# Performance work log

Measured on AMD Instinct MI355X. Metric: run time of the kernel, lower is better.

The kernel has to match this reference:

```python
import jax, jax.numpy as jnp
import numpy as np

EPS = 1e-12  # torch F.normalize clamps the norm at 1e-12

def _l2norm(v, axis):
    n = jnp.sqrt(jnp.sum(v * v, axis=axis, keepdims=True))
    return v / jnp.maximum(n, EPS)

def setup_inputs() -> dict:
    key = jax.random.key(0)
    k1, k2, k3, k4 = jax.random.split(key, 4)
    N, C, H, W, K = 64, 64, 64, 64, 128
    alpha = 1.0
    x = jax.random.normal(k1, (N, C, H, W), dtype=jnp.float32)
    centroids = jax.random.uniform(k2, (K, C), dtype=jnp.float32)
    # conv is initialized from centroids (2*alpha*c, -alpha*||c||) but is an
    # independent parameter after init; keep the init relationship for realism.
    conv_w = 2.0 * alpha * centroids
    conv_b = -alpha * jnp.sqrt(jnp.sum(centroids * centroids, axis=1))
    return {"x": x, "centroids": centroids, "conv_w": conv_w, "conv_b": conv_b}

def reference(x, centroids, conv_w, conv_b):
    N, C, H, W = x.shape
    K = centroids.shape[0]
    # L2-normalize descriptors along channel dim
    xn = _l2norm(x, axis=1)                                   # [N,C,H,W]
    # 1x1 conv == per-pixel linear map C->K
    logits = jnp.einsum('nchw,kc->nkhw', xn, conv_w) + conv_b[None, :, None, None]
    sa = jax.nn.softmax(logits.reshape(N, K, H * W), axis=1)  # [N,K,HW]
    xf = xn.reshape(N, C, H * W)                              # [N,C,HW]
    # vlad[n,k,c] = sum_l sa[n,k,l] * (xf[n,c,l] - centroids[k,c])
    #            = (sa @ xf^T)[n,k,c] - sum_l sa[n,k,l] * centroids[k,c]
    vlad = jnp.einsum('nkl,ncl->nkc', sa, xf) - sa.sum(axis=-1)[:, :, None] * centroids[None]
    vlad = _l2norm(vlad, axis=2)            # intra-normalization per cluster
    vlad = vlad.reshape(N, K * C)
    vlad = _l2norm(vlad, axis=1)            # global L2 normalization
    return vlad
```

## Files before the change

### kernel.cpp

```cpp
#include <hip/hip_runtime.h>
#include <math.h>

#define NIMG   64
#define CDIM   64
#define HWPX   4096
#define KCL    128
#define TL     64
#define SHIFT  10.0f
#define RSQRT128 0.08838834764831845f

#define XP_S 72
#define XC_S 72
#define PH_S 72

typedef __attribute__((ext_vector_type(8))) short short8;
typedef __attribute__((ext_vector_type(4))) float f32x4;

#define MFMA(a, b, c) __builtin_amdgcn_mfma_f32_16x16x32_bf16((a), (b), (c), 0, 0, 0)

#define PERM_HI16 0x07060302u

#define BAR() do {                                          \
    asm volatile("s_waitcnt lgkmcnt(0)" ::: "memory");      \
    __builtin_amdgcn_s_barrier();                           \
    __builtin_amdgcn_sched_barrier(0);                      \
} while (0)

template <int NP>
__global__ __launch_bounds__(256, 2)
void netvlad_main(const float* __restrict__ x,
                  const float* __restrict__ conv_w,
                  const float* __restrict__ conv_b,
                  float* __restrict__ vout,
                  float* __restrict__ asout,
                  int use_atomic)
{
    constexpr int PIXPART = HWPX / NP;
    constexpr int NCHUNK  = PIXPART / TL;

    __shared__ __align__(16) short xp_hi[2][TL * XP_S], xp_lo[2][TL * XP_S];
    __shared__ __align__(16) short xc[2][CDIM * XC_S];
    __shared__ __align__(16) short ph[KCL * PH_S];
    __shared__ __align__(8) float2 redA2[2][4 * 32];
    __shared__ __align__(8) float2 sumP2[2][4 * 32];

    const int t   = threadIdx.x;
    const int w   = t >> 6;
    const int l   = t & 63;
    const int l15 = l & 15, l4 = l >> 4;
    const int n    = blockIdx.x / NP;
    const int part = blockIdx.x - n * NP;
    const int q    = t & 31;
    const int sg   = t >> 5;
    const int p0   = (q & 15) + ((q & 16) << 1);
    const int xslot = ((q >> 4) << 5) + 2 * (q & 15);

    short8 wh[2][2], wl[2][2];
    #pragma unroll
    for (int kt = 0; kt < 2; ++kt) {
        const int krow = (2 * w + kt) * 16 + l15;
        #pragma unroll
        for (int ks = 0; ks < 2; ++ks) {
            const float4* wp = (const float4*)(conv_w + krow * CDIM + ks * 32 + l4 * 8);
            float4 wa = wp[0], wb = wp[1];
            float wv[8] = {wa.x, wa.y, wa.z, wa.w, wb.x, wb.y, wb.z, wb.w};
            #pragma unroll
            for (int j = 0; j < 8; ++j) {
                unsigned u = __builtin_bit_cast(unsigned, wv[j]);
                wh[kt][ks][j] = (short)(u >> 16);
                float hf = __builtin_bit_cast(float, u & 0xffff0000u);
                wl[kt][ks][j] = (short)(__builtin_bit_cast(unsigned, wv[j] - hf) >> 16);
            }
        }
    }
    float cbr[2][4];
    #pragma unroll
    for (int kt = 0; kt < 2; ++kt)
        #pragma unroll
        for (int i = 0; i < 4; ++i)
            cbr[kt][i] = conv_b[(2 * w + kt) * 16 + l4 * 4 + i] - SHIFT;

    f32x4 acc2[2][4];
    #pragma unroll
    for (int a = 0; a < 2; ++a)
        #pragma unroll
        for (int b = 0; b < 4; ++b) acc2[a][b] = (f32x4)0.0f;
    float asr[2][4];
    #pragma unroll
    for (int a = 0; a < 2; ++a)
        #pragma unroll
        for (int i = 0; i < 4; ++i) asr[a][i] = 0.f;

    const float* xbase = x + (size_t)n * CDIM * HWPX + part * PIXPART;

    float xv0[8], xv1[8];

    float e[2][4][4];
    float rnv[4];

    #define LOADX(OFF) do {                                                 \
        _Pragma("unroll")                                                   \
        for (int j = 0; j < 8; ++j) {                                       \
            xv0[j] = xbase[(sg * 8 + j) * HWPX + (OFF) + p0];               \
            xv1[j] = xbase[(sg * 8 + j) * HWPX + (OFF) + p0 + 16];          \
        }                                                                   \
    } while (0)

    auto stage = [&](int buf) {
        float ssq0 = 0.f, ssq1 = 0.f;
        #pragma unroll
        for (int j = 0; j < 8; ++j) {
            ssq0 += xv0[j] * xv0[j];
            ssq1 += xv1[j] * xv1[j];
        }
        ssq0 += __shfl_xor(ssq0, 32);
        ssq1 += __shfl_xor(ssq1, 32);
        if (l < 32) redA2[buf][w * 32 + q] = make_float2(ssq0, ssq1);

        {
            unsigned uh[4], ul[4];
            #pragma unroll
            for (int jp = 0; jp < 4; ++jp) {
                const unsigned u0 = __builtin_bit_cast(unsigned, xv0[2 * jp]);
                const unsigned u1 = __builtin_bit_cast(unsigned, xv0[2 * jp + 1]);
                uh[jp] = __builtin_amdgcn_perm(u1, u0, PERM_HI16);
                const float h0 = __builtin_bit_cast(float, u0 & 0xffff0000u);
                const float h1 = __builtin_bit_cast(float, u1 & 0xffff0000u);
                const unsigned lo0 = __builtin_bit_cast(unsigned, xv0[2 * jp] - h0);
                const unsigned lo1 = __builtin_bit_cast(unsigned, xv0[2 * jp + 1] - h1);
                ul[jp] = __builtin_amdgcn_perm(lo1, lo0, PERM_HI16);
            }
            *(uint4*)&xp_hi[buf][p0 * XP_S + sg * 8] = make_uint4(uh[0], uh[1], uh[2], uh[3]);
            *(uint4*)&xp_lo[buf][p0 * XP_S + sg * 8] = make_uint4(ul[0], ul[1], ul[2], ul[3]);
        }
        {
            unsigned uh[4], ul[4];
            #pragma unroll
            for (int jp = 0; jp < 4; ++jp) {
                const unsigned u0 = __builtin_bit_cast(unsigned, xv1[2 * jp]);
                const unsigned u1 = __builtin_bit_cast(unsigned, xv1[2 * jp + 1]);
                uh[jp] = __builtin_amdgcn_perm(u1, u0, PERM_HI16);
                const float h0 = __builtin_bit_cast(float, u0 & 0xffff0000u);
                const float h1 = __builtin_bit_cast(float, u1 & 0xffff0000u);
                const unsigned lo0 = __builtin_bit_cast(unsigned, xv1[2 * jp] - h0);
                const unsigned lo1 = __builtin_bit_cast(unsigned, xv1[2 * jp + 1] - h1);
                ul[jp] = __builtin_amdgcn_perm(lo1, lo0, PERM_HI16);
            }
            *(uint4*)&xp_hi[buf][(p0 + 16) * XP_S + sg * 8] = make_uint4(uh[0], uh[1], uh[2], uh[3]);
            *(uint4*)&xp_lo[buf][(p0 + 16) * XP_S + sg * 8] = make_uint4(ul[0], ul[1], ul[2], ul[3]);
        }

        #pragma unroll
        for (int j = 0; j < 8; ++j) {
            unsigned pk;
            asm("v_cvt_pk_bf16_f32 %0, %1, %2"
                : "=v"(pk) : "v"(xv0[j]), "v"(xv1[j]));
            *(unsigned*)&xc[buf][(sg * 8 + j) * XC_S + xslot] = pk;
        }
    };

    auto mm1_sec = [&](int b) {
        f32x4 a1[2][4];
        #pragma unroll
        for (int a = 0; a < 2; ++a)
            #pragma unroll
            for (int c = 0; c < 4; ++c) a1[a][c] = (f32x4)0.0f;
        #pragma unroll
        for (int ks = 0; ks < 2; ++ks) {
            #pragma unroll
            for (int pt = 0; pt < 4; ++pt) {
                short8 bh = *(short8*)&xp_hi[b][(pt * 16 + l15) * XP_S + ks * 32 + l4 * 8];
                short8 bl = *(short8*)&xp_lo[b][(pt * 16 + l15) * XP_S + ks * 32 + l4 * 8];
                #pragma unroll
                for (int kt = 0; kt < 2; ++kt) {
                    a1[kt][pt] = MFMA(wh[kt][ks], bh, a1[kt][pt]);
                    a1[kt][pt] = MFMA(wh[kt][ks], bl, a1[kt][pt]);
                    a1[kt][pt] = MFMA(wl[kt][ks], bh, a1[kt][pt]);
                }
            }
        }

        float2 ra0 = redA2[b][l15],           ra1 = redA2[b][32 + l15];
        float2 ra2 = redA2[b][64 + l15],      ra3 = redA2[b][96 + l15];
        float2 rb0 = redA2[b][16 + l15],      rb1 = redA2[b][48 + l15];
        float2 rb2 = redA2[b][80 + l15],      rb3 = redA2[b][112 + l15];
        rnv[0] = 1.0f / fmaxf(sqrtf((ra0.x + ra1.x) + (ra2.x + ra3.x)), 1e-12f);
        rnv[1] = 1.0f / fmaxf(sqrtf((ra0.y + ra1.y) + (ra2.y + ra3.y)), 1e-12f);
        rnv[2] = 1.0f / fmaxf(sqrtf((rb0.x + rb1.x) + (rb2.x + rb3.x)), 1e-12f);
        rnv[3] = 1.0f / fmaxf(sqrtf((rb0.y + rb1.y) + (rb2.y + rb3.y)), 1e-12f);

        float sp[4] = {0.f, 0.f, 0.f, 0.f};
        #pragma unroll
        for (int kt = 0; kt < 2; ++kt)
            #pragma unroll
            for (int pt = 0; pt < 4; ++pt)
                #pragma unroll
                for (int i = 0; i < 4; ++i) {
                    float ev = __expf(fmaf(a1[kt][pt][i], rnv[pt], cbr[kt][i]));
                    e[kt][pt][i] = ev;
                    sp[pt] += ev;
                }
        #pragma unroll
        for (int pt = 0; pt < 4; ++pt) {
            sp[pt] += __shfl_xor(sp[pt], 16);
            sp[pt] += __shfl_xor(sp[pt], 32);
        }
        if (l4 == 0)      sumP2[b][w * 32 + l15]      = make_float2(sp[0], sp[1]);
        else if (l4 == 1) sumP2[b][w * 32 + 16 + l15] = make_float2(sp[2], sp[3]);
    };

    auto ph_mm2 = [&](int pb) {
        float2 q0 = sumP2[pb][l15],       q1 = sumP2[pb][32 + l15];
        float2 q2 = sumP2[pb][64 + l15],  q3 = sumP2[pb][96 + l15];
        float2 r0 = sumP2[pb][16 + l15],  r1 = sumP2[pb][48 + l15];
        float2 r2 = sumP2[pb][80 + l15],  r3 = sumP2[pb][112 + l15];
        float rden[4], rdn2[4];
        rden[0] = 1.0f / ((q0.x + q1.x) + (q2.x + q3.x));
        rden[1] = 1.0f / ((q0.y + q1.y) + (q2.y + q3.y));
        rden[2] = 1.0f / ((r0.x + r1.x) + (r2.x + r3.x));
        rden[3] = 1.0f / ((r0.y + r1.y) + (r2.y + r3.y));
        #pragma unroll
        for (int pt = 0; pt < 4; ++pt) rdn2[pt] = rden[pt] * rnv[pt];

        #pragma unroll
        for (int kt = 0; kt < 2; ++kt)
            #pragma unroll
            for (int i = 0; i < 4; ++i) {
                const int row = (2 * w + kt) * 16 + l4 * 4 + i;
                const float e0 = e[kt][0][i], e1 = e[kt][1][i];
                const float e2 = e[kt][2][i], e3 = e[kt][3][i];
                asr[kt][i] = fmaf(e0, rden[0], asr[kt][i]);
                asr[kt][i] = fmaf(e1, rden[1], asr[kt][i]);
                asr[kt][i] = fmaf(e2, rden[2], asr[kt][i]);
                asr[kt][i] = fmaf(e3, rden[3], asr[kt][i]);
                const float p0f = e0 * rdn2[0], p1f = e1 * rdn2[1];
                const float p2f = e2 * rdn2[2], p3f = e3 * rdn2[3];
                unsigned pk01, pk23;
                asm("v_cvt_pk_bf16_f32 %0, %1, %2" : "=v"(pk01) : "v"(p0f), "v"(p1f));
                asm("v_cvt_pk_bf16_f32 %0, %1, %2" : "=v"(pk23) : "v"(p2f), "v"(p3f));
                *(unsigned*)&ph[row * PH_S + 2 * l15]      = pk01;
                *(unsigned*)&ph[row * PH_S + 32 + 2 * l15] = pk23;
            }

        short8 xh2[4][2];
        #pragma unroll
        for (int ct = 0; ct < 4; ++ct)
            #pragma unroll
            for (int hh = 0; hh < 2; ++hh)
                xh2[ct][hh] = *(short8*)&xc[pb][(ct * 16 + l15) * XC_S + hh * 32 + l4 * 8];
        #pragma unroll
        for (int kt = 0; kt < 2; ++kt) {
            short8 ah0 = *(short8*)&ph[((2 * w + kt) * 16 + l15) * PH_S + l4 * 8];
            short8 ah1 = *(short8*)&ph[((2 * w + kt) * 16 + l15) * PH_S + 32 + l4 * 8];
            #pragma unroll
            for (int ct = 0; ct < 4; ++ct) {
                acc2[kt][ct] = MFMA(ah0, xh2[ct][0], acc2[kt][ct]);
                acc2[kt][ct] = MFMA(ah1, xh2[ct][1], acc2[kt][ct]);
            }
        }
    };

    LOADX(0);
    stage(0);
    if (NCHUNK > 1) LOADX(TL);
    BAR();
    if (NCHUNK > 1) stage(1);
    if (NCHUNK > 2) LOADX(2 * TL);
    mm1_sec(0);
    BAR();

    for (int ch = 1; ch < NCHUNK; ++ch) {
        ph_mm2((ch - 1) & 1);
        BAR();
        if (ch + 1 < NCHUNK) stage((ch + 1) & 1);
        if (ch + 2 < NCHUNK) LOADX((ch + 2) * TL);
        mm1_sec(ch & 1);
        BAR();
    }
    ph_mm2((NCHUNK - 1) & 1);
    #undef LOADX

    float* vg = use_atomic ? vout + (size_t)n * KCL * CDIM
                           : vout + (size_t)blockIdx.x * KCL * CDIM;
    #pragma unroll
    for (int kt = 0; kt < 2; ++kt)
        #pragma unroll
        for (int ct = 0; ct < 4; ++ct)
            #pragma unroll
            for (int i = 0; i < 4; ++i) {
                const int row = (2 * w + kt) * 16 + l4 * 4 + i;
                const int col = ct * 16 + l15;
                if (use_atomic) atomicAdd(&vg[row * CDIM + col], acc2[kt][ct][i]);
                else            vg[row * CDIM + col] = acc2[kt][ct][i];
            }

    #pragma unroll
    for (int kt = 0; kt < 2; ++kt)
        #pragma unroll
        for (int i = 0; i < 4; ++i) {
            float v = asr[kt][i];
            v += __shfl_xor(v, 1); v += __shfl_xor(v, 2);
            v += __shfl_xor(v, 4); v += __shfl_xor(v, 8);
            if (l15 == 0) {
                const int row = (2 * w + kt) * 16 + l4 * 4 + i;
                if (use_atomic) atomicAdd(&asout[n * KCL + row], v);
                else            asout[blockIdx.x * KCL + row] = v;
            }
        }
}

template <int NPARTS>
__global__ __launch_bounds__(256)
void netvlad_finalize(const float* __restrict__ vpart,
                      const float* __restrict__ aspart,
                      const float* __restrict__ cent,
                      float* __restrict__ out)
{
    const int t = threadIdx.x;
    const int n  = blockIdx.x >> 3;
    const int kg = blockIdx.x & 7;
    const int k  = kg * 16 + (t >> 4);
    const int c0 = (t & 15) * 4;

    float vsum[4] = {0.f, 0.f, 0.f, 0.f};
    float av = 0.f;
    #pragma unroll
    for (int pt = 0; pt < NPARTS; ++pt) {
        const float* vg = vpart + (((size_t)n * NPARTS + pt) * KCL + k) * CDIM + c0;
        float4 a = *(const float4*)vg;
        vsum[0] += a.x; vsum[1] += a.y; vsum[2] += a.z; vsum[3] += a.w;
        av += aspart[(n * NPARTS + pt) * KCL + k];
    }

    float4 cq = *(const float4*)(cent + k * CDIM + c0);
    float cc[4] = {cq.x, cq.y, cq.z, cq.w};
    float ss = 0.f;
    #pragma unroll
    for (int j = 0; j < 4; ++j) {
        vsum[j] -= av * cc[j];
        ss += vsum[j] * vsum[j];
    }
    ss += __shfl_xor(ss, 1); ss += __shfl_xor(ss, 2);
    ss += __shfl_xor(ss, 4); ss += __shfl_xor(ss, 8);
    const float s = (1.0f / fmaxf(sqrtf(ss), 1e-12f)) * RSQRT128;

    float4 o;
    o.x = vsum[0] * s; o.y = vsum[1] * s; o.z = vsum[2] * s; o.w = vsum[3] * s;
    *(float4*)(out + (size_t)n * KCL * CDIM + k * CDIM + c0) = o;
}

extern "C" void kernel_launch(void* const* d_in, const int* in_sizes, int n_in,
                              void* d_out, int out_size, void* d_ws, size_t ws_size,
                              hipStream_t stream) {
    const float* x     = (const float*)d_in[0];
    const float* cent  = (const float*)d_in[1];
    const float* convw = (const float*)d_in[2];
    const float* convb = (const float*)d_in[3];
    float* out = (float*)d_out;

    const size_t need8 = (size_t)NIMG * 8 * (KCL * CDIM + KCL) * sizeof(float);

    if (ws_size >= need8) {
        float* vws  = (float*)d_ws;
        float* asws = vws + (size_t)NIMG * 8 * KCL * CDIM;
        netvlad_main<8><<<dim3(NIMG * 8), dim3(256), 0, stream>>>(
            x, convw, convb, vws, asws, 0);
        netvlad_finalize<8><<<dim3(NIMG * 8), dim3(256), 0, stream>>>(
            vws, asws, cent, out);
    } else {
        float* vws  = (float*)d_ws;
        float* asws = vws + (size_t)NIMG * KCL * CDIM;
        const size_t zb = (size_t)NIMG * (KCL * CDIM + KCL) * sizeof(float);
        hipMemsetAsync(d_ws, 0, zb, stream);
        netvlad_main<8><<<dim3(NIMG * 8), dim3(256), 0, stream>>>(
            x, convw, convb, vws, asws, 1);
        netvlad_finalize<1><<<dim3(NIMG * 8), dim3(256), 0, stream>>>(
            vws, asws, cent, out);
    }
}
```

Measured before the change: 123.7 us.

## Fuse finalize into main kernel using last-block-per-image atomic counter

Replaces the separate finalize launch with a per-image atomic counter: the last of the NP blocks for each image sums the partial VLAD and assignment-sum buffers, subtracts centroids, normalizes, and writes the output. This removes one kernel launch and its inter-kernel gap, at the cost of a small counter memset and a serialized tail where 64 blocks each do eight groups of finalize work. It relies on threadfence and cross-block visibility of partial results.

Result: slower. 176.8 us (+42.9%).

```diff
diff --git a/kernel.cpp b/kernel.cpp
--- a/kernel.cpp
+++ b/kernel.cpp
@@ -26,14 +26,16 @@
     __builtin_amdgcn_sched_barrier(0);                      \
 } while (0)
 
-template <int NP>
+template <int NP, int FUSED>
 __global__ __launch_bounds__(256, 2)
 void netvlad_main(const float* __restrict__ x,
                   const float* __restrict__ conv_w,
                   const float* __restrict__ conv_b,
+                  const float* __restrict__ cent,
                   float* __restrict__ vout,
                   float* __restrict__ asout,
-                  int use_atomic)
+                  int* __restrict__ counters,
+                  float* __restrict__ outp)
 {
     constexpr int PIXPART = HWPX / NP;
     constexpr int NCHUNK  = PIXPART / TL;
@@ -280,8 +282,8 @@
     ph_mm2((NCHUNK - 1) & 1);
     #undef LOADX
 
-    float* vg = use_atomic ? vout + (size_t)n * KCL * CDIM
-                           : vout + (size_t)blockIdx.x * KCL * CDIM;
+    float* vg = FUSED ? vout + (size_t)blockIdx.x * KCL * CDIM
+                      : vout + (size_t)n * KCL * CDIM;
     #pragma unroll
     for (int kt = 0; kt < 2; ++kt)
         #pragma unroll
@@ -290,8 +292,8 @@
             for (int i = 0; i < 4; ++i) {
                 const int row = (2 * w + kt) * 16 + l4 * 4 + i;
                 const int col = ct * 16 + l15;
-                if (use_atomic) atomicAdd(&vg[row * CDIM + col], acc2[kt][ct][i]);
-                else            vg[row * CDIM + col] = acc2[kt][ct][i];
+                if (FUSED) vg[row * CDIM + col] = acc2[kt][ct][i];
+                else       atomicAdd(&vg[row * CDIM + col], acc2[kt][ct][i]);
             }
 
     #pragma unroll
@@ -303,10 +305,52 @@
             v += __shfl_xor(v, 4); v += __shfl_xor(v, 8);
             if (l15 == 0) {
                 const int row = (2 * w + kt) * 16 + l4 * 4 + i;
-                if (use_atomic) atomicAdd(&asout[n * KCL + row], v);
-                else            asout[blockIdx.x * KCL + row] = v;
-            }
-        }
+                if (FUSED) asout[blockIdx.x * KCL + row] = v;
+                else       atomicAdd(&asout[n * KCL + row], v);
+            }
+        }
+
+    if (!FUSED) return;
+
+    __syncthreads();
+    __shared__ int lastFlag;
+    if (t == 0) {
+        __threadfence();
+        lastFlag = (atomicAdd(&counters[n], 1) == NP - 1) ? 1 : 0;
+    }
+    __syncthreads();
+    if (!lastFlag) return;
+    __threadfence();
+
+    const int kk = t >> 4;
+    const int c0 = (t & 15) * 4;
+    #pragma unroll
+    for (int kg = 0; kg < 8; ++kg) {
+        const int k = kg * 16 + kk;
+        float vs[4] = {0.f, 0.f, 0.f, 0.f};
+        float av = 0.f;
+        #pragma unroll
+        for (int pt = 0; pt < NP; ++pt) {
+            const float* vg2 = vout + (((size_t)n * NP + pt) * KCL + k) * CDIM + c0;
+            float4 a = *(const float4*)vg2;
+            vs[0] += a.x; vs[1] += a.y; vs[2] += a.z; vs[3] += a.w;
+            av += asout[(n * NP + pt) * KCL + k];
+        }
+        float4 cq = *(const float4*)(cent + k * CDIM + c0);
+        float cc[4] = {cq.x, cq.y, cq.z, cq.w};
+        float ss = 0.f;
+        #pragma unroll
+        for (int j = 0; j < 4; ++j) {
+            vs[j] -= av * cc[j];
+            ss += vs[j] * vs[j];
+        }
+        ss += __shfl_xor(ss, 1); ss += __shfl_xor(ss, 2);
+        ss += __shfl_xor(ss, 4); ss += __shfl_xor(ss, 8);
+        const float s = (1.0f / fmaxf(sqrtf(ss), 1e-12f)) * RSQRT128;
+        float4 o;
+        o.x = vs[0] * s; o.y = vs[1] * s; o.z = vs[2] * s; o.w = vs[3] * s;
+        *(float4*)(outp + (size_t)n * KCL * CDIM + k * CDIM + c0) = o;
+    }
 }
 
 template <int NPARTS>
@@ -358,22 +402,23 @@
     const float* convb = (const float*)d_in[3];
     float* out = (float*)d_out;
 
-    const size_t need8 = (size_t)NIMG * 8 * (KCL * CDIM + KCL) * sizeof(float);
-
-    if (ws_size >= need8) {
-        float* vws  = (float*)d_ws;
+    const size_t part_floats = (size_t)NIMG * 8 * (KCL * CDIM + KCL);
+    const size_t need_fused  = 1024 + part_floats * sizeof(float);
+
+    if (ws_size >= need_fused) {
+        int*   counters = (int*)d_ws;
+        float* vws  = (float*)((char*)d_ws + 1024);
         float* asws = vws + (size_t)NIMG * 8 * KCL * CDIM;
-        netvlad_main<8><<<dim3(NIMG * 8), dim3(256), 0, stream>>>(
-            x, convw, convb, vws, asws, 0);
-        netvlad_finalize<8><<<dim3(NIMG * 8), dim3(256), 0, stream>>>(
-            vws, asws, cent, out);
+        hipMemsetAsync(d_ws, 0, 1024, stream);
+        netvlad_main<8, 1><<<dim3(NIMG * 8), dim3(256), 0, stream>>>(
+            x, convw, convb, cent, vws, asws, counters, out);
     } else {
         float* vws  = (float*)d_ws;
         float* asws = vws + (size_t)NIMG * KCL * CDIM;
         const size_t zb = (size_t)NIMG * (KCL * CDIM + KCL) * sizeof(float);
         hipMemsetAsync(d_ws, 0, zb, stream);
-        netvlad_main<8><<<dim3(NIMG * 8), dim3(256), 0, stream>>>(
-            x, convw, convb, vws, asws, 1);
+        netvlad_main<8, 0><<<dim3(NIMG * 8), dim3(256), 0, stream>>>(
+            x, convw, convb, cent, vws, asws, nullptr, out);
         netvlad_finalize<1><<<dim3(NIMG * 8), dim3(256), 0, stream>>>(
             vws, asws, cent, out);
     }
```
